# Optimization experiments

Measured on AMD Instinct MI355X. Metric: run time of the kernel, lower is better.

The kernel has to match this reference:

```python
import jax, jax.numpy as jnp
import numpy as np

H = 768          # hidden_size
V = 32000        # vocab_size
NUM_GATES = 5    # none/dontcare/ptr/yes/no
PAD = 0          # pad_token_id


def setup_inputs() -> dict:
    key = jax.random.key(0)
    ks = jax.random.split(key, 10)
    B, S, J, Ls = 16, 512, 30, 4
    max_len = 8
    sc = 1.0 / np.sqrt(H).astype(np.float32)
    E = jax.random.normal(ks[0], (V, H), jnp.float32) * sc
    E = E.at[PAD].set(0.0)  # padding_idx row is zero
    return dict(
        input_ids=jax.random.randint(ks[1], (B, S), 0, V),
        encoder_output=jax.random.normal(ks[2], (B, S, H), jnp.float32),
        hidden=jax.random.normal(ks[3], (1, B, H), jnp.float32),
        input_masks=jnp.ones((B, S), jnp.int32),  # 1 = valid token
        slot=jax.random.randint(ks[4], (J, Ls), 0, V),
        max_len=max_len,
        E=E,
        W_ih=jax.random.normal(ks[5], (3 * H, H), jnp.float32) * sc,
        W_hh=jax.random.normal(ks[6], (3 * H, H), jnp.float32) * sc,
        b_ih=jnp.zeros((3 * H,), jnp.float32),
        b_hh=jnp.zeros((3 * H,), jnp.float32),
        W_gen=jax.random.normal(ks[7], (3 * H, 1), jnp.float32) * sc,
        b_gen=jnp.zeros((1,), jnp.float32),
        W_gate=jax.random.normal(ks[8], (H, NUM_GATES), jnp.float32) * sc,
        b_gate=jnp.zeros((NUM_GATES,), jnp.float32),
    )


def gru_step(x, h, W_ih, W_hh, b_ih, b_hh):
    # PyTorch GRUCell math
    gi = x @ W_ih.T + b_ih
    gh = h @ W_hh.T + b_hh
    ir, iz, inn = jnp.split(gi, 3, axis=-1)
    hr, hz, hn = jnp.split(gh, 3, axis=-1)
    r = jax.nn.sigmoid(ir + hr)
    z = jax.nn.sigmoid(iz + hz)
    n = jnp.tanh(inn + r * hn)
    return (1.0 - z) * n + z * h


def reference(input_ids, encoder_output, hidden, input_masks, slot, max_len,
              E, W_ih, W_hh, b_ih, b_hh, W_gen, b_gen, W_gate, b_gate):
    B, S, Hd = encoder_output.shape
    J = slot.shape[0]
    mask = input_masks != 1                         # True -> masked (pad)
    slot_e = E[slot].sum(axis=1)                    # [J, H]
    BJ = B * J
    # parallel decoding: flat index = b*J + j (matches repeat/repeat_interleave)
    w = jnp.tile(slot_e, (B, 1))                    # [BJ, H]
    h = jnp.repeat(hidden[0], J, axis=0)            # [BJ, H]
    enc = jnp.repeat(encoder_output, J, axis=0)     # [BJ, S, H]
    ids = jnp.repeat(input_ids, J, axis=0)          # [BJ, S]
    msk = jnp.repeat(mask, J, axis=0)               # [BJ, S]
    rows = jnp.arange(BJ)

    def step(carry, _):
        w, h = carry
        h = gru_step(w, h, W_ih, W_hh, b_ih, b_hh)                    # [BJ, H]
        attn_e = jnp.einsum('bsh,bh->bs', enc, h)                     # [BJ, S]
        attn_e = jnp.where(msk, -1e9, attn_e)
        attn_history = jax.nn.softmax(attn_e, axis=-1)                # [BJ, S]
        attn_vocab = jax.nn.softmax(h @ E.T, axis=-1)                 # [BJ, V]
        context = jnp.einsum('bs,bsh->bh', attn_history, enc)         # [BJ, H]
        p_gen = jax.nn.sigmoid(
            jnp.concatenate([w, h, context], -1) @ W_gen + b_gen)     # [BJ, 1]
        ptr = jnp.zeros_like(attn_vocab).at[rows[:, None], ids].add(attn_history)
        p_final = p_gen * attn_vocab + (1.0 - p_gen) * ptr            # [BJ, V]
        w_next = E[jnp.argmax(p_final, axis=-1)]                      # greedy (teacher=None)
        return (w_next, h), (p_final, context)

    (_, _), (points, contexts) = jax.lax.scan(step, (w, h), None, length=max_len)
    gate_logit = contexts[0] @ W_gate + b_gate                        # gate from step k==0
    all_points = points.transpose(1, 0, 2).reshape(B, J, max_len, V)
    all_gates = gate_logit.reshape(B, J, NUM_GATES)
    return all_points, all_gates
```

## Files before the change

### kernel.cpp

```cpp
#include <hip/hip_runtime.h>
#include <cstdint>
#include <cstddef>

#define HDIM 768
#define VOCAB 32000
#define NGATES 5
#define NJ 30
#define NB 16
#define NS 512
#define NBJ (NB*NJ)
#define G3 2304
#define PR 608
#define NBV 250

typedef _Float16 f16;
typedef _Float16 f16x8 __attribute__((ext_vector_type(8)));
typedef float f32x4 __attribute__((ext_vector_type(4)));

#define GLOBAL_AS __attribute__((address_space(1)))
#define LDS_AS    __attribute__((address_space(3)))

__global__ void k_cast(const float* __restrict__ src, f16* __restrict__ dst, int n) {
    for (int i = blockIdx.x*256 + threadIdx.x; i < n; i += gridDim.x*256)
        dst[i] = (f16)src[i];
}

__global__ void k_cast_split(const float* __restrict__ src, f16* __restrict__ hi,
                             f16* __restrict__ lo, int n) {
    for (int i = blockIdx.x*256 + threadIdx.x; i < n; i += gridDim.x*256) {
        float v = src[i];
        f16 h = (f16)v;
        hi[i] = h;
        lo[i] = (f16)(v - (float)h);
    }
}

__global__ void k_init_state(const float* __restrict__ E, const int* __restrict__ slot,
                             const float* __restrict__ hidden,
                             f16* __restrict__ w_hi, f16* __restrict__ w_lo,
                             float* __restrict__ h,
                             f16* __restrict__ h_hi, f16* __restrict__ h_lo) {
    int total = NBJ*HDIM;
    for (int i = blockIdx.x*256 + threadIdx.x; i < total; i += gridDim.x*256) {
        int hh = i % HDIM, row = i / HDIM;
        int b = row / NJ, j = row % NJ;
        float s = 0.f;
        #pragma unroll
        for (int l = 0; l < 4; ++l) s += E[(long)slot[j*4+l]*HDIM + hh];
        f16 sh = (f16)s;
        w_hi[i] = sh; w_lo[i] = (f16)(s - (float)sh);
        float hv = hidden[b*HDIM + hh];
        h[i] = hv;
        f16 hh16 = (f16)hv;
        h_hi[i] = hh16; h_lo[i] = (f16)(hv - (float)hh16);
    }
}

__launch_bounds__(256)
__global__ void k_gemm(const f16* __restrict__ Ah, const f16* __restrict__ Al,
                       const f16* __restrict__ Bh, const f16* __restrict__ Bl,
                       float* __restrict__ Cf, f16* __restrict__ Ch,
                       float* __restrict__ psum,
                       int M, long ldc, long coff, int kdim, int nspan,
                       long aBS, long bBS, long cBS) {
    __shared__ f16 a_lds[8][128][8];
    __shared__ f16 b_lds[8][128][8];
    __shared__ float sbuf[2][128];

    const int tid = threadIdx.x;
    const int z = blockIdx.z;
    const int m0 = blockIdx.x*128, n0 = blockIdx.y*128;
    const int w = tid >> 6, lane = tid & 63;
    const int wm = (w >> 1)*64, wn = (w & 1)*64;
    const int lr = lane & 15, lg = lane >> 4;

    f32x4 acc[4][4] = {};

    for (int sp = 0; sp < nspan; ++sp) {
        const f16* Ap = ((sp < 2) ? Ah : Al) + (long)z*aBS;
        const f16* Bp = ((sp == 1) ? Bl : Bh) + (long)z*bBS;
        for (int kc = 0; kc < kdim; kc += 64) {
            #pragma unroll
            for (int i = 0; i < 4; ++i) {
                const int idx = w*4 + i;
                const int c = idx >> 1;
                const int rl = (idx & 1)*64 + lane;
                const f16* ga = Ap + (long)(m0 + rl)*kdim + kc + c*8;
                const f16* gb = Bp + (long)(n0 + rl)*kdim + kc + c*8;
                __builtin_amdgcn_global_load_lds(
                    (const GLOBAL_AS unsigned int*)ga,
                    (LDS_AS unsigned int*)((char*)&a_lds[0][0][0] + idx*1024), 16, 0, 0);
                __builtin_amdgcn_global_load_lds(
                    (const GLOBAL_AS unsigned int*)gb,
                    (LDS_AS unsigned int*)((char*)&b_lds[0][0][0] + idx*1024), 16, 0, 0);
            }
            __syncthreads();
            #pragma unroll
            for (int kk = 0; kk < 2; ++kk) {
                const int c = kk*4 + lg;
                f16x8 af[4], bf[4];
                #pragma unroll
                for (int mi = 0; mi < 4; ++mi) af[mi] = *(const f16x8*)&a_lds[c][wm + mi*16 + lr][0];
                #pragma unroll
                for (int nf = 0; nf < 4; ++nf) bf[nf] = *(const f16x8*)&b_lds[c][wn + nf*16 + lr][0];
                #pragma unroll
                for (int mi = 0; mi < 4; ++mi)
                    #pragma unroll
                    for (int nf = 0; nf < 4; ++nf)
                        acc[mi][nf] = __builtin_amdgcn_mfma_f32_16x16x32_f16(af[mi], bf[nf], acc[mi][nf], 0, 0, 0);
            }
            __syncthreads();
        }
    }

    if (Ch != nullptr) {
        f16* Cb = Ch + (long)z*cBS + coff;
        #pragma unroll
        for (int mi = 0; mi < 4; ++mi)
            #pragma unroll
            for (int nf = 0; nf < 4; ++nf) {
                int col = n0 + wn + nf*16 + lr;
                int rowb = m0 + wm + mi*16 + lg*4;
                #pragma unroll
                for (int r = 0; r < 4; ++r) {
                    int row = rowb + r;
                    if (row < M) Cb[(long)row*ldc + col] = (f16)acc[mi][nf][r];
                }
            }
    } else {
        float* Cb = Cf + (long)z*cBS + coff;
        #pragma unroll
        for (int mi = 0; mi < 4; ++mi)
            #pragma unroll
            for (int nf = 0; nf < 4; ++nf) {
                int col = n0 + wn + nf*16 + lr;
                int rowb = m0 + wm + mi*16 + lg*4;
                #pragma unroll
                for (int r = 0; r < 4; ++r) {
                    int row = rowb + r;
                    if (row < M) Cb[(long)row*ldc + col] = acc[mi][nf][r];
                }
            }
    }

    if (psum != nullptr) {
        #pragma unroll
        for (int mi = 0; mi < 4; ++mi) {
            #pragma unroll
            for (int r = 0; r < 4; ++r) {
                float s = 0.f;
                #pragma unroll
                for (int nf = 0; nf < 4; ++nf) s += expf((float)(f16)acc[mi][nf][r]);
                s += __shfl_xor(s, 1); s += __shfl_xor(s, 2);
                s += __shfl_xor(s, 4); s += __shfl_xor(s, 8);
                if (lr == 0) sbuf[w & 1][wm + mi*16 + lg*4 + r] = s;
            }
        }
        __syncthreads();
        if (tid < 128)
            psum[(long)blockIdx.y*512 + m0 + tid] = sbuf[0][tid] + sbuf[1][tid];
    }
}

__global__ void k_gru_elem(const float* __restrict__ gi, const float* __restrict__ gh,
                           const float* __restrict__ bih, const float* __restrict__ bhh,
                           float* __restrict__ h, f16* __restrict__ h_hi, f16* __restrict__ h_lo) {
    int total = NBJ*HDIM;
    for (int i = blockIdx.x*256 + threadIdx.x; i < total; i += gridDim.x*256) {
        int c = i % HDIM; long row = i / HDIM;
        long base = row*G3;
        float r = gi[base + c]        + bih[c]        + gh[base + c]        + bhh[c];
        float z = gi[base + 768 + c]  + bih[768 + c]  + gh[base + 768 + c]  + bhh[768 + c];
        float hn = gh[base + 1536 + c] + bhh[1536 + c];
        float in_ = gi[base + 1536 + c] + bih[1536 + c];
        r = 1.f/(1.f + expf(-r));
        z = 1.f/(1.f + expf(-z));
        float n = tanhf(in_ + r*hn);
        float hv = (1.f - z)*n + z*h[i];
        h[i] = hv;
        f16 hh16 = (f16)hv;
        h_hi[i] = hh16; h_lo[i] = (f16)(hv - (float)hh16);
    }
}

__launch_bounds__(256)
__global__ void k_attn(const float* __restrict__ h, const float* __restrict__ enc,
                       float* __restrict__ attn_e) {
    __shared__ float h_lds[NJ][64];
    __shared__ float e_lds[64][65];
    const int b = blockIdx.x, st = blockIdx.y;
    const int s0 = st*64;
    const int tid = threadIdx.x;
    const int s = tid & 63, jg = tid >> 6;
    float acc[8] = {};
    for (int kc = 0; kc < HDIM; kc += 64) {
        for (int idx = tid; idx < NJ*64; idx += 256) {
            int j = idx >> 6, k = idx & 63;
            h_lds[j][k] = h[((long)(b*NJ + j))*HDIM + kc + k];
        }
        #pragma unroll
        for (int i = 0; i < 4; ++i) {
            int id = tid + i*256;
            int ss = id >> 4, kq = (id & 15)*4;
            float4 v = *(const float4*)&enc[((long)b*NS + s0 + ss)*HDIM + kc + kq];
            e_lds[ss][kq+0] = v.x; e_lds[ss][kq+1] = v.y;
            e_lds[ss][kq+2] = v.z; e_lds[ss][kq+3] = v.w;
        }
        __syncthreads();
        for (int k = 0; k < 64; ++k) {
            float e = e_lds[s][k];
            #pragma unroll
            for (int i = 0; i < 8; ++i) {
                int j = jg + i*4;
                if (j < NJ) acc[i] += h_lds[j][k]*e;
            }
        }
        __syncthreads();
    }
    #pragma unroll
    for (int i = 0; i < 8; ++i) {
        int j = jg + i*4;
        if (j < NJ) attn_e[((long)(b*NJ + j))*NS + s0 + s] = acc[i];
    }
}

__launch_bounds__(256)
__global__ void k_softmax_s(float* __restrict__ ae, const int* __restrict__ masks) {
    const int row = blockIdx.x, tid = threadIdx.x;
    const int b = row / NJ;
    __shared__ float red[256];
    float x0 = ae[(long)row*NS + tid];
    float x1 = ae[(long)row*NS + tid + 256];
    if (masks[b*NS + tid]       != 1) x0 = -1e9f;
    if (masks[b*NS + tid + 256] != 1) x1 = -1e9f;
    red[tid] = fmaxf(x0, x1); __syncthreads();
    for (int o = 128; o > 0; o >>= 1) { if (tid < o) red[tid] = fmaxf(red[tid], red[tid+o]); __syncthreads(); }
    float m = red[0]; __syncthreads();
    float e0 = expf(x0 - m), e1 = expf(x1 - m);
    red[tid] = e0 + e1; __syncthreads();
    for (int o = 128; o > 0; o >>= 1) { if (tid < o) red[tid] += red[tid+o]; __syncthreads(); }
    float inv = 1.f/red[0];
    ae[(long)row*NS + tid]       = e0*inv;
    ae[(long)row*NS + tid + 256] = e1*inv;
}

__launch_bounds__(256)
__global__ void k_context(const float* __restrict__ ah, const float* __restrict__ enc,
                          float* __restrict__ ctx) {
    __shared__ float a_lds[NJ][64];
    const int b = blockIdx.x, ht = blockIdx.y;
    const int hh = ht*128 + (threadIdx.x & 127);
    const int jg = threadIdx.x >> 7;
    float acc[15] = {};
    for (int sc = 0; sc < NS; sc += 64) {
        for (int idx = threadIdx.x; idx < NJ*64; idx += 256) {
            int j = idx >> 6, s = idx & 63;
            a_lds[j][s] = ah[((long)(b*NJ + j))*NS + sc + s];
        }
        __syncthreads();
        for (int s = 0; s < 64; ++s) {
            float e = enc[((long)b*NS + sc + s)*HDIM + hh];
            #pragma unroll
            for (int i = 0; i < 15; ++i) acc[i] += a_lds[jg + i*2][s]*e;
        }
        __syncthreads();
    }
    #pragma unroll
    for (int i = 0; i < 15; ++i) ctx[((long)(b*NJ + jg + i*2))*HDIM + hh] = acc[i];
}

__launch_bounds__(64)
__global__ void k_pgen(const f16* __restrict__ w_hi, const f16* __restrict__ w_lo,
                       const float* __restrict__ h,
                       const float* __restrict__ ctx, const float* __restrict__ Wgen,
                       const float* __restrict__ bgen, const float* __restrict__ Wgate,
                       const float* __restrict__ bgate, float* __restrict__ pgen,
                       float* __restrict__ out_gates, int do_gate) {
    const int row = blockIdx.x, lane = threadIdx.x;
    float acc = 0.f;
    for (int x = lane; x < HDIM; x += 64) {
        float wv = (float)w_hi[(long)row*HDIM + x] + (float)w_lo[(long)row*HDIM + x];
        acc += wv                          * Wgen[x];
        acc += h[(long)row*HDIM + x]       * Wgen[768 + x];
        acc += ctx[(long)row*HDIM + x]     * Wgen[1536 + x];
    }
    for (int o = 32; o > 0; o >>= 1) acc += __shfl_down(acc, o);
    if (lane == 0) pgen[row] = 1.f/(1.f + expf(-(acc + bgen[0])));
    if (do_gate) {
        for (int g = 0; g < NGATES; ++g) {
            float a = 0.f;
            for (int x = lane; x < HDIM; x += 64) a += ctx[(long)row*HDIM + x]*Wgate[x*NGATES + g];
            for (int o = 32; o > 0; o >>= 1) a += __shfl_down(a, o);
            if (lane == 0) out_gates[row*NGATES + g] = a + bgate[g];
        }
    }
}

__launch_bounds__(256)
__global__ void k_scale(const f16* __restrict__ l16, float* __restrict__ out,
                        long ldrow, long coff,
                        const float* __restrict__ psum, const float* __restrict__ pgen,
                        unsigned long long* __restrict__ pamax) {
    const int row = blockIdx.x, c = blockIdx.y, tid = threadIdx.x;
    __shared__ float red[256];
    float s = 0.f;
    for (int nb = tid; nb < NBV; nb += 256) s += psum[(long)nb*512 + row];
    red[tid] = s; __syncthreads();
    for (int o = 128; o > 0; o >>= 1) { if (tid < o) red[tid] += red[tid+o]; __syncthreads(); }
    const float scale = pgen[row] / red[0];

    const f16* lb = l16 + (long)row*VOCAB;
    float* ob = out + (long)row*ldrow + coff;
    const int v0 = c*4000;
    float bv = -1.f; int bi = 0x7FFFFFFF;
    for (int v = v0 + tid; v < v0 + 4000; v += 256) {
        float val = scale*expf((float)lb[v]);
        ob[v] = val;
        if (val > bv) { bv = val; bi = v; }
    }
    __shared__ float rv[256]; __shared__ int ri[256];
    rv[tid] = bv; ri[tid] = bi; __syncthreads();
    for (int o = 128; o > 0; o >>= 1) {
        if (tid < o) {
            float v2 = rv[tid+o]; int i2 = ri[tid+o];
            if (v2 > rv[tid] || (v2 == rv[tid] && i2 < ri[tid])) { rv[tid] = v2; ri[tid] = i2; }
        }
        __syncthreads();
    }
    if (tid == 0)
        pamax[(long)row*8 + c] = ((unsigned long long)__float_as_uint(rv[0]) << 32)
                               | (unsigned long long)(0xFFFFFFFFu - (unsigned)ri[0]);
}

__launch_bounds__(256)
__global__ void k_scatter(float* __restrict__ pts, long ldrow, long coff,
                          const int* __restrict__ ids, const float* __restrict__ ah,
                          const float* __restrict__ pgen,
                          const unsigned long long* __restrict__ pamax,
                          const float* __restrict__ E,
                          f16* __restrict__ w_hi, f16* __restrict__ w_lo) {
    const int row = blockIdx.x, tid = threadIdx.x;
    const int b = row / NJ;
    float* base = pts + (long)row*ldrow + coff;
    const float cp = 1.f - pgen[row];
    float sv = -1.f; int si = 0x7FFFFFFF;
    for (int ss = tid; ss < NS; ss += 256) {
        int id = ids[(long)b*NS + ss];
        float add = cp * ah[(long)row*NS + ss];
        float old = atomicAdd(base + id, add);
        float cand = old + add;
        if (cand > sv || (cand == sv && id < si)) { sv = cand; si = id; }
    }
    __shared__ float rv[256]; __shared__ int ri[256];
    rv[tid] = sv; ri[tid] = si; __syncthreads();
    for (int o = 128; o > 0; o >>= 1) {
        if (tid < o) {
            float v2 = rv[tid+o]; int i2 = ri[tid+o];
            if (v2 > rv[tid] || (v2 == rv[tid] && i2 < ri[tid])) { rv[tid] = v2; ri[tid] = i2; }
        }
        __syncthreads();
    }
    __shared__ int bidx;
    if (tid == 0) {
        float vv = rv[0]; int ii = ri[0];
        #pragma unroll
        for (int cc = 0; cc < 8; ++cc) {
            unsigned long long pk = pamax[(long)row*8 + cc];
            float pv = __uint_as_float((unsigned)(pk >> 32));
            int pi = (int)(0xFFFFFFFFu - (unsigned)(pk & 0xFFFFFFFFu));
            if (pv > vv || (pv == vv && pi < ii)) { vv = pv; ii = pi; }
        }
        bidx = ii;
    }
    __syncthreads();
    const int idx = bidx;
    for (int x = tid; x < HDIM; x += 256) {
        float ev = E[(long)idx*HDIM + x];
        f16 eh = (f16)ev;
        w_hi[(long)row*HDIM + x] = eh;
        w_lo[(long)row*HDIM + x] = (f16)(ev - (float)eh);
    }
}

extern "C" void kernel_launch(void* const* d_in, const int* in_sizes, int n_in,
                              void* d_out, int out_size, void* d_ws, size_t ws_size,
                              hipStream_t stream) {
    const int*   input_ids = (const int*)  d_in[0];
    const float* enc       = (const float*)d_in[1];
    const float* hidden    = (const float*)d_in[2];
    const int*   masks     = (const int*)  d_in[3];
    const int*   slot      = (const int*)  d_in[4];
    const float* E     = (const float*)d_in[6];
    const float* Wih   = (const float*)d_in[7];
    const float* Whh   = (const float*)d_in[8];
    const float* bih   = (const float*)d_in[9];
    const float* bhh   = (const float*)d_in[10];
    const float* Wgen  = (const float*)d_in[11];
    const float* bgen  = (const float*)d_in[12];
    const float* Wgate = (const float*)d_in[13];
    const float* bgate = (const float*)d_in[14];

    const int ml = (out_size / NBJ - NGATES) / VOCAB;
    float* out = (float*)d_out;
    float* gates_out = out + (long)NBJ*ml*VOCAB;

    char* ws = (char*)d_ws;
    auto carve = [&](size_t bytes) { char* p = ws; ws += (bytes + 255) & ~(size_t)255; return p; };
    f16*   E16   = (f16*)carve((size_t)VOCAB*HDIM*2);
    f16*   WH2   = (f16*)carve((size_t)2*G3*HDIM*2);
    f16*   WL2   = (f16*)carve((size_t)2*G3*HDIM*2);
    f16*   SH    = (f16*)carve((size_t)2*PR*HDIM*2);
    f16*   SL    = (f16*)carve((size_t)2*PR*HDIM*2);
    float* gigh  = (float*)carve((size_t)2*NBJ*G3*4);
    float* hbuf  = (float*)carve((size_t)NBJ*HDIM*4);
    float* ae    = (float*)carve((size_t)NBJ*NS*4);
    float* ctx   = (float*)carve((size_t)NBJ*HDIM*4);
    f16*   l16   = (f16*)carve((size_t)NBJ*VOCAB*2);
    float* pgen  = (float*)carve((size_t)NBJ*4);
    float* ps    = (float*)carve((size_t)NBV*512*4);
    unsigned long long* pamax = (unsigned long long*)carve((size_t)NBJ*8*8);

    f16* WihH = WH2;  f16* WihL = WL2;
    f16* wH = SH;     f16* wL = SL;
    f16* hH = SH + (size_t)PR*HDIM;
    f16* hL = SL + (size_t)PR*HDIM;

    k_cast<<<8192, 256, 0, stream>>>(E, E16, VOCAB*HDIM);
    k_cast_split<<<2048, 256, 0, stream>>>(Wih, WihH, WihL, G3*HDIM);
    k_cast_split<<<2048, 256, 0, stream>>>(Whh, WH2 + (size_t)G3*HDIM, WL2 + (size_t)G3*HDIM, G3*HDIM);
    k_init_state<<<1440, 256, 0, stream>>>(E, slot, hidden, wH, wL, hbuf, hH, hL);

    const long ldrow = (long)ml*VOCAB;
    for (int t = 0; t < ml; ++t) {
        k_gemm<<<dim3(4, 18, 2), 256, 0, stream>>>(wH, wL, WihH, WihL, gigh, nullptr, nullptr,
            NBJ, (long)G3, 0, HDIM, 3, (long)PR*HDIM, (long)G3*HDIM, (long)NBJ*G3);
        k_gru_elem<<<1440, 256, 0, stream>>>(gigh, gigh + (size_t)NBJ*G3, bih, bhh, hbuf, hH, hL);
        k_attn<<<dim3(NB, 8), 256, 0, stream>>>(hbuf, enc, ae);
        k_softmax_s<<<NBJ, 256, 0, stream>>>(ae, masks);
        k_context<<<dim3(NB, 6), 256, 0, stream>>>(ae, enc, ctx);
        k_pgen<<<NBJ, 64, 0, stream>>>(wH, wL, hbuf, ctx, Wgen, bgen, Wgate, bgate,
                                       pgen, gates_out, t == 0 ? 1 : 0);
        k_gemm<<<dim3(4, NBV, 1), 256, 0, stream>>>(hH, hL, E16, nullptr, nullptr, l16, ps,
            NBJ, (long)VOCAB, 0, HDIM, 1, 0, 0, 0);
        k_scale<<<dim3(NBJ, 8), 256, 0, stream>>>(l16, out, ldrow, (long)t*VOCAB, ps, pgen, pamax);
        k_scatter<<<NBJ, 256, 0, stream>>>(out, ldrow, (long)t*VOCAB, input_ids, ae, pgen,
                                           pamax, E, wH, wL);
    }
}
```

Baseline: 3.409 ms.

## Fuse all per-step kernels into one persistent kernel with grid barriers

Replaces the sequence of roughly nine kernel launches per decode step, plus the setup casts, with a single persistent kernel. It is sized to the occupancy-limited grid and separates phases with an atomic-counter global barrier. Work items (GEMM tiles, attention tiles, rows) are distributed round-robin over the resident blocks, and LDS is shared through a union. The goal is to remove launch overhead and inter-kernel gaps. In exchange, every phase is limited to the resident block count, each phase costs a global barrier spin, and the scale and scatter kernels are merged into one row loop.

```diff
diff --git a/kernel.cpp b/kernel.cpp
--- a/kernel.cpp
+++ b/kernel.cpp
@@ -14,62 +14,40 @@
 #define NBV 250
 
 typedef _Float16 f16;
+typedef _Float16 f16x4 __attribute__((ext_vector_type(4)));
 typedef _Float16 f16x8 __attribute__((ext_vector_type(8)));
 typedef float f32x4 __attribute__((ext_vector_type(4)));
 
 #define GLOBAL_AS __attribute__((address_space(1)))
 #define LDS_AS    __attribute__((address_space(3)))
 
-__global__ void k_cast(const float* __restrict__ src, f16* __restrict__ dst, int n) {
-    for (int i = blockIdx.x*256 + threadIdx.x; i < n; i += gridDim.x*256)
-        dst[i] = (f16)src[i];
+union SharedU {
+    struct { f16 a[8][128][8]; f16 b[8][128][8]; float sbuf[2][128]; } g;
+    struct { float h[NJ][64]; float e[64][65]; } at;
+    struct { float a[NJ][64]; } cx;
+    struct { float red[256]; float rv[256]; int ri[256]; } rd;
+};
+
+__device__ __forceinline__ void gbar(unsigned* bar, unsigned nblk, unsigned& ph) {
+    __syncthreads();
+    ph += nblk;
+    if (threadIdx.x == 0) {
+        __threadfence();
+        __hip_atomic_fetch_add(bar, 1u, __ATOMIC_RELEASE, __HIP_MEMORY_SCOPE_AGENT);
+        while (__hip_atomic_load(bar, __ATOMIC_ACQUIRE, __HIP_MEMORY_SCOPE_AGENT) < ph)
+            __builtin_amdgcn_s_sleep(2);
+        __threadfence();
+    }
+    __syncthreads();
 }
 
-__global__ void k_cast_split(const float* __restrict__ src, f16* __restrict__ hi,
-                             f16* __restrict__ lo, int n) {
-    for (int i = blockIdx.x*256 + threadIdx.x; i < n; i += gridDim.x*256) {
-        float v = src[i];
-        f16 h = (f16)v;
-        hi[i] = h;
-        lo[i] = (f16)(v - (float)h);
-    }
-}
-
-__global__ void k_init_state(const float* __restrict__ E, const int* __restrict__ slot,
-                             const float* __restrict__ hidden,
-                             f16* __restrict__ w_hi, f16* __restrict__ w_lo,
-                             float* __restrict__ h,
-                             f16* __restrict__ h_hi, f16* __restrict__ h_lo) {
-    int total = NBJ*HDIM;
-    for (int i = blockIdx.x*256 + threadIdx.x; i < total; i += gridDim.x*256) {
-        int hh = i % HDIM, row = i / HDIM;
-        int b = row / NJ, j = row % NJ;
-        float s = 0.f;
-        #pragma unroll
-        for (int l = 0; l < 4; ++l) s += E[(long)slot[j*4+l]*HDIM + hh];
-        f16 sh = (f16)s;
-        w_hi[i] = sh; w_lo[i] = (f16)(s - (float)sh);
-        float hv = hidden[b*HDIM + hh];
-        h[i] = hv;
-        f16 hh16 = (f16)hv;
-        h_hi[i] = hh16; h_lo[i] = (f16)(hv - (float)hh16);
-    }
-}
-
-__launch_bounds__(256)
-__global__ void k_gemm(const f16* __restrict__ Ah, const f16* __restrict__ Al,
-                       const f16* __restrict__ Bh, const f16* __restrict__ Bl,
-                       float* __restrict__ Cf, f16* __restrict__ Ch,
-                       float* __restrict__ psum,
-                       int M, long ldc, long coff, int kdim, int nspan,
-                       long aBS, long bBS, long cBS) {
-    __shared__ f16 a_lds[8][128][8];
-    __shared__ f16 b_lds[8][128][8];
-    __shared__ float sbuf[2][128];
-
+__device__ __forceinline__ void gemm_tile(
+        const f16* __restrict__ Ah, const f16* __restrict__ Al,
+        const f16* __restrict__ Bh, const f16* __restrict__ Bl,
+        float* __restrict__ Cf, f16* __restrict__ Ch, float* __restrict__ psum,
+        int M, long ldc, int kdim, int nspan, int bx, int by, SharedU* sh) {
     const int tid = threadIdx.x;
-    const int z = blockIdx.z;
-    const int m0 = blockIdx.x*128, n0 = blockIdx.y*128;
+    const int m0 = bx*128, n0 = by*128;
     const int w = tid >> 6, lane = tid & 63;
     const int wm = (w >> 1)*64, wn = (w & 1)*64;
     const int lr = lane & 15, lg = lane >> 4;
@@ -77,8 +55,8 @@
     f32x4 acc[4][4] = {};
 
     for (int sp = 0; sp < nspan; ++sp) {
-        const f16* Ap = ((sp < 2) ? Ah : Al) + (long)z*aBS;
-        const f16* Bp = ((sp == 1) ? Bl : Bh) + (long)z*bBS;
+        const f16* Ap = (sp < 2) ? Ah : Al;
+        const f16* Bp = (sp == 1) ? Bl : Bh;
         for (int kc = 0; kc < kdim; kc += 64) {
             #pragma unroll
             for (int i = 0; i < 4; ++i) {
@@ -89,10 +67,10 @@
                 const f16* gb = Bp + (long)(n0 + rl)*kdim + kc + c*8;
                 __builtin_amdgcn_global_load_lds(
                     (const GLOBAL_AS unsigned int*)ga,
-                    (LDS_AS unsigned int*)((char*)&a_lds[0][0][0] + idx*1024), 16, 0, 0);
+                    (LDS_AS unsigned int*)((char*)&sh->g.a[0][0][0] + idx*1024), 16, 0, 0);
                 __builtin_amdgcn_global_load_lds(
                     (const GLOBAL_AS unsigned int*)gb,
-                    (LDS_AS unsigned int*)((char*)&b_lds[0][0][0] + idx*1024), 16, 0, 0);
+                    (LDS_AS unsigned int*)((char*)&sh->g.b[0][0][0] + idx*1024), 16, 0, 0);
             }
             __syncthreads();
             #pragma unroll
@@ -100,9 +78,9 @@
                 const int c = kk*4 + lg;
                 f16x8 af[4], bf[4];
                 #pragma unroll
-                for (int mi = 0; mi < 4; ++mi) af[mi] = *(const f16x8*)&a_lds[c][wm + mi*16 + lr][0];
-                #pragma unroll
-                for (int nf = 0; nf < 4; ++nf) bf[nf] = *(const f16x8*)&b_lds[c][wn + nf*16 + lr][0];
+                for (int mi = 0; mi < 4; ++mi) af[mi] = *(const f16x8*)&sh->g.a[c][wm + mi*16 + lr][0];
+                #pragma unroll
+                for (int nf = 0; nf < 4; ++nf) bf[nf] = *(const f16x8*)&sh->g.b[c][wn + nf*16 + lr][0];
                 #pragma unroll
                 for (int mi = 0; mi < 4; ++mi)
                     #pragma unroll
@@ -114,7 +92,6 @@
     }
 
     if (Ch != nullptr) {
-        f16* Cb = Ch + (long)z*cBS + coff;
         #pragma unroll
         for (int mi = 0; mi < 4; ++mi)
             #pragma unroll
@@ -124,11 +101,10 @@
                 #pragma unroll
                 for (int r = 0; r < 4; ++r) {
                     int row = rowb + r;
-                    if (row < M) Cb[(long)row*ldc + col] = (f16)acc[mi][nf][r];
+                    if (row < M) Ch[(long)row*ldc + col] = (f16)acc[mi][nf][r];
                 }
             }
     } else {
-        float* Cb = Cf + (long)z*cBS + coff;
         #pragma unroll
         for (int mi = 0; mi < 4; ++mi)
             #pragma unroll
@@ -138,7 +114,7 @@
                 #pragma unroll
                 for (int r = 0; r < 4; ++r) {
                     int row = rowb + r;
-                    if (row < M) Cb[(long)row*ldc + col] = acc[mi][nf][r];
+                    if (row < M) Cf[(long)row*ldc + col] = acc[mi][nf][r];
                 }
             }
     }
@@ -153,232 +129,274 @@
                 for (int nf = 0; nf < 4; ++nf) s += expf((float)(f16)acc[mi][nf][r]);
                 s += __shfl_xor(s, 1); s += __shfl_xor(s, 2);
                 s += __shfl_xor(s, 4); s += __shfl_xor(s, 8);
-                if (lr == 0) sbuf[w & 1][wm + mi*16 + lg*4 + r] = s;
+                if (lr == 0) sh->g.sbuf[w & 1][wm + mi*16 + lg*4 + r] = s;
             }
         }
         __syncthreads();
-        if (tid < 128)
-            psum[(long)blockIdx.y*512 + m0 + tid] = sbuf[0][tid] + sbuf[1][tid];
+        if (tid < 128) psum[(long)by*512 + m0 + tid] = sh->g.sbuf[0][tid] + sh->g.sbuf[1][tid];
+        __syncthreads();
     }
 }
 
-__global__ void k_gru_elem(const float* __restrict__ gi, const float* __restrict__ gh,
-                           const float* __restrict__ bih, const float* __restrict__ bhh,
-                           float* __restrict__ h, f16* __restrict__ h_hi, f16* __restrict__ h_lo) {
-    int total = NBJ*HDIM;
-    for (int i = blockIdx.x*256 + threadIdx.x; i < total; i += gridDim.x*256) {
-        int c = i % HDIM; long row = i / HDIM;
-        long base = row*G3;
-        float r = gi[base + c]        + bih[c]        + gh[base + c]        + bhh[c];
-        float z = gi[base + 768 + c]  + bih[768 + c]  + gh[base + 768 + c]  + bhh[768 + c];
-        float hn = gh[base + 1536 + c] + bhh[1536 + c];
-        float in_ = gi[base + 1536 + c] + bih[1536 + c];
-        r = 1.f/(1.f + expf(-r));
-        z = 1.f/(1.f + expf(-z));
-        float n = tanhf(in_ + r*hn);
-        float hv = (1.f - z)*n + z*h[i];
-        h[i] = hv;
-        f16 hh16 = (f16)hv;
-        h_hi[i] = hh16; h_lo[i] = (f16)(hv - (float)hh16);
-    }
-}
-
-__launch_bounds__(256)
-__global__ void k_attn(const float* __restrict__ h, const float* __restrict__ enc,
-                       float* __restrict__ attn_e) {
-    __shared__ float h_lds[NJ][64];
-    __shared__ float e_lds[64][65];
-    const int b = blockIdx.x, st = blockIdx.y;
-    const int s0 = st*64;
-    const int tid = threadIdx.x;
-    const int s = tid & 63, jg = tid >> 6;
-    float acc[8] = {};
-    for (int kc = 0; kc < HDIM; kc += 64) {
-        for (int idx = tid; idx < NJ*64; idx += 256) {
-            int j = idx >> 6, k = idx & 63;
-            h_lds[j][k] = h[((long)(b*NJ + j))*HDIM + kc + k];
-        }
-        #pragma unroll
-        for (int i = 0; i < 4; ++i) {
-            int id = tid + i*256;
-            int ss = id >> 4, kq = (id & 15)*4;
-            float4 v = *(const float4*)&enc[((long)b*NS + s0 + ss)*HDIM + kc + kq];
-            e_lds[ss][kq+0] = v.x; e_lds[ss][kq+1] = v.y;
-            e_lds[ss][kq+2] = v.z; e_lds[ss][kq+3] = v.w;
-        }
-        __syncthreads();
-        for (int k = 0; k < 64; ++k) {
-            float e = e_lds[s][k];
+__launch_bounds__(256, 2)
+__global__ void k_mega(const int* __restrict__ ids, const float* __restrict__ enc,
+                       const float* __restrict__ hidden, const int* __restrict__ masks,
+                       const int* __restrict__ slot, const float* __restrict__ E,
+                       const float* __restrict__ Wih, const float* __restrict__ Whh,
+                       const float* __restrict__ bih, const float* __restrict__ bhh,
+                       const float* __restrict__ Wgen, const float* __restrict__ bgen,
+                       const float* __restrict__ Wgate, const float* __restrict__ bgate,
+                       float* __restrict__ out, float* __restrict__ gates_out, int ml,
+                       f16* __restrict__ E16, f16* __restrict__ WH2, f16* __restrict__ WL2,
+                       f16* __restrict__ SH, f16* __restrict__ SL,
+                       float* __restrict__ gigh, float* __restrict__ hbuf,
+                       float* __restrict__ ae, float* __restrict__ ctx,
+                       f16* __restrict__ l16, float* __restrict__ pgen,
+                       float* __restrict__ ps, unsigned* __restrict__ bar, int nblk) {
+    __shared__ SharedU sh;
+    __shared__ int s_bidx;
+    unsigned ph = 0;
+
+    const int blk = blockIdx.x, tid = threadIdx.x;
+    f16* wH = SH;                       f16* wL = SL;
+    f16* hH = SH + (size_t)PR*HDIM;     f16* hL = SL + (size_t)PR*HDIM;
+    float* gi = gigh;                   float* gh = gigh + (size_t)NBJ*G3;
+    const long ldrow = (long)ml*VOCAB;
+
+    {
+        const long nE = (long)VOCAB*HDIM;
+        for (long i = (long)(blk*256 + tid)*4; i < nE; i += (long)nblk*256*4) {
+            float4 v = *(const float4*)&E[i];
+            f16x4 o = { (f16)v.x, (f16)v.y, (f16)v.z, (f16)v.w };
+            *(f16x4*)&E16[i] = o;
+        }
+        const long nW = (long)G3*HDIM;
+        for (long i = (long)(blk*256 + tid)*4; i < nW; i += (long)nblk*256*4) {
+            float4 a = *(const float4*)&Wih[i];
+            f16x4 h = { (f16)a.x, (f16)a.y, (f16)a.z, (f16)a.w };
+            f16x4 l = { (f16)(a.x-(float)h[0]), (f16)(a.y-(float)h[1]),
+                        (f16)(a.z-(float)h[2]), (f16)(a.w-(float)h[3]) };
+            *(f16x4*)&WH2[i] = h; *(f16x4*)&WL2[i] = l;
+            float4 b = *(const float4*)&Whh[i];
+            f16x4 h2 = { (f16)b.x, (f16)b.y, (f16)b.z, (f16)b.w };
+            f16x4 l2 = { (f16)(b.x-(float)h2[0]), (f16)(b.y-(float)h2[1]),
+                         (f16)(b.z-(float)h2[2]), (f16)(b.w-(float)h2[3]) };
+            *(f16x4*)&WH2[nW + i] = h2; *(f16x4*)&WL2[nW + i] = l2;
+        }
+        for (int i = blk*256 + tid; i < NBJ*HDIM; i += nblk*256) {
+            int hh = i % HDIM, row = i / HDIM;
+            int b = row / NJ, j = row % NJ;
+            float s = 0.f;
+            #pragma unroll
+            for (int l = 0; l < 4; ++l) s += E[(long)slot[j*4+l]*HDIM + hh];
+            f16 sh16 = (f16)s;
+            wH[i] = sh16; wL[i] = (f16)(s - (float)sh16);
+            float hv = hidden[b*HDIM + hh];
+            hbuf[i] = hv;
+            f16 hh16 = (f16)hv;
+            hH[i] = hh16; hL[i] = (f16)(hv - (float)hh16);
+        }
+    }
+    gbar(bar, nblk, ph);
+
+    for (int t = 0; t < ml; ++t) {
+        for (int bi = blk; bi < 144; bi += nblk) {
+            int z = bi / 72, r = bi % 72, bx = r & 3, by = r >> 2;
+            gemm_tile(z ? hH : wH, z ? hL : wL,
+                      WH2 + (size_t)z*G3*HDIM, WL2 + (size_t)z*G3*HDIM,
+                      z ? gh : gi, nullptr, nullptr,
+                      NBJ, (long)G3, HDIM, 3, bx, by, &sh);
+        }
+        gbar(bar, nblk, ph);
+
+        for (int i = blk*256 + tid; i < NBJ*HDIM; i += nblk*256) {
+            int c = i % HDIM; long row = i / HDIM;
+            long base = row*G3;
+            float r = gi[base + c]         + bih[c]        + gh[base + c]         + bhh[c];
+            float z = gi[base + 768 + c]   + bih[768 + c]  + gh[base + 768 + c]   + bhh[768 + c];
+            float hn  = gh[base + 1536 + c] + bhh[1536 + c];
+            float in_ = gi[base + 1536 + c] + bih[1536 + c];
+            r = 1.f/(1.f + expf(-r));
+            z = 1.f/(1.f + expf(-z));
+            float n = tanhf(in_ + r*hn);
+            float hv = (1.f - z)*n + z*hbuf[i];
+            hbuf[i] = hv;
+            f16 hh16 = (f16)hv;
+            hH[i] = hh16; hL[i] = (f16)(hv - (float)hh16);
+        }
+        gbar(bar, nblk, ph);
+
+        for (int bi = blk; bi < 128; bi += nblk) {
+            __syncthreads();
+            const int b = bi >> 3, s0 = (bi & 7)*64;
+            const int s = tid & 63, jg = tid >> 6;
+            float acc[8] = {};
+            for (int kc = 0; kc < HDIM; kc += 64) {
+                for (int idx = tid; idx < NJ*64; idx += 256) {
+                    int j = idx >> 6, k = idx & 63;
+                    sh.at.h[j][k] = hbuf[((long)(b*NJ + j))*HDIM + kc + k];
+                }
+                #pragma unroll
+                for (int i = 0; i < 4; ++i) {
+                    int id = tid + i*256;
+                    int ss = id >> 4, kq = (id & 15)*4;
+                    float4 v = *(const float4*)&enc[((long)b*NS + s0 + ss)*HDIM + kc + kq];
+                    sh.at.e[ss][kq+0] = v.x; sh.at.e[ss][kq+1] = v.y;
+                    sh.at.e[ss][kq+2] = v.z; sh.at.e[ss][kq+3] = v.w;
+                }
+                __syncthreads();
+                for (int k = 0; k < 64; ++k) {
+                    float e = sh.at.e[s][k];
+                    #pragma unroll
+                    for (int i = 0; i < 8; ++i) {
+                        int j = jg + i*4;
+                        if (j < NJ) acc[i] += sh.at.h[j][k]*e;
+                    }
+                }
+                __syncthreads();
+            }
             #pragma unroll
             for (int i = 0; i < 8; ++i) {
                 int j = jg + i*4;
-                if (j < NJ) acc[i] += h_lds[j][k]*e;
-            }
-        }
-        __syncthreads();
-    }
-    #pragma unroll
-    for (int i = 0; i < 8; ++i) {
-        int j = jg + i*4;
-        if (j < NJ) attn_e[((long)(b*NJ + j))*NS + s0 + s] = acc[i];
-    }
-}
-
-__launch_bounds__(256)
-__global__ void k_softmax_s(float* __restrict__ ae, const int* __restrict__ masks) {
-    const int row = blockIdx.x, tid = threadIdx.x;
-    const int b = row / NJ;
-    __shared__ float red[256];
-    float x0 = ae[(long)row*NS + tid];
-    float x1 = ae[(long)row*NS + tid + 256];
-    if (masks[b*NS + tid]       != 1) x0 = -1e9f;
-    if (masks[b*NS + tid + 256] != 1) x1 = -1e9f;
-    red[tid] = fmaxf(x0, x1); __syncthreads();
-    for (int o = 128; o > 0; o >>= 1) { if (tid < o) red[tid] = fmaxf(red[tid], red[tid+o]); __syncthreads(); }
-    float m = red[0]; __syncthreads();
-    float e0 = expf(x0 - m), e1 = expf(x1 - m);
-    red[tid] = e0 + e1; __syncthreads();
-    for (int o = 128; o > 0; o >>= 1) { if (tid < o) red[tid] += red[tid+o]; __syncthreads(); }
-    float inv = 1.f/red[0];
-    ae[(long)row*NS + tid]       = e0*inv;
-    ae[(long)row*NS + tid + 256] = e1*inv;
-}
-
-__launch_bounds__(256)
-__global__ void k_context(const float* __restrict__ ah, const float* __restrict__ enc,
-                          float* __restrict__ ctx) {
-    __shared__ float a_lds[NJ][64];
-    const int b = blockIdx.x, ht = blockIdx.y;
-    const int hh = ht*128 + (threadIdx.x & 127);
-    const int jg = threadIdx.x >> 7;
-    float acc[15] = {};
-    for (int sc = 0; sc < NS; sc += 64) {
-        for (int idx = threadIdx.x; idx < NJ*64; idx += 256) {
-            int j = idx >> 6, s = idx & 63;
-            a_lds[j][s] = ah[((long)(b*NJ + j))*NS + sc + s];
-        }
-        __syncthreads();
-        for (int s = 0; s < 64; ++s) {
-            float e = enc[((long)b*NS + sc + s)*HDIM + hh];
-            #pragma unroll
-            for (int i = 0; i < 15; ++i) acc[i] += a_lds[jg + i*2][s]*e;
-        }
-        __syncthreads();
-    }
-    #pragma unroll
-    for (int i = 0; i < 15; ++i) ctx[((long)(b*NJ + jg + i*2))*HDIM + hh] = acc[i];
-}
-
-__launch_bounds__(64)
-__global__ void k_pgen(const f16* __restrict__ w_hi, const f16* __restrict__ w_lo,
-                       const float* __restrict__ h,
-                       const float* __restrict__ ctx, const float* __restrict__ Wgen,
-                       const float* __restrict__ bgen, const float* __restrict__ Wgate,
-                       const float* __restrict__ bgate, float* __restrict__ pgen,
-                       float* __restrict__ out_gates, int do_gate) {
-    const int row = blockIdx.x, lane = threadIdx.x;
-    float acc = 0.f;
-    for (int x = lane; x < HDIM; x += 64) {
-        float wv = (float)w_hi[(long)row*HDIM + x] + (float)w_lo[(long)row*HDIM + x];
-        acc += wv                          * Wgen[x];
-        acc += h[(long)row*HDIM + x]       * Wgen[768 + x];
-        acc += ctx[(long)row*HDIM + x]     * Wgen[1536 + x];
-    }
-    for (int o = 32; o > 0; o >>= 1) acc += __shfl_down(acc, o);
-    if (lane == 0) pgen[row] = 1.f/(1.f + expf(-(acc + bgen[0])));
-    if (do_gate) {
-        for (int g = 0; g < NGATES; ++g) {
-            float a = 0.f;
-            for (int x = lane; x < HDIM; x += 64) a += ctx[(long)row*HDIM + x]*Wgate[x*NGATES + g];
-            for (int o = 32; o > 0; o >>= 1) a += __shfl_down(a, o);
-            if (lane == 0) out_gates[row*NGATES + g] = a + bgate[g];
-        }
-    }
-}
-
-__launch_bounds__(256)
-__global__ void k_scale(const f16* __restrict__ l16, float* __restrict__ out,
-                        long ldrow, long coff,
-                        const float* __restrict__ psum, const float* __restrict__ pgen,
-                        unsigned long long* __restrict__ pamax) {
-    const int row = blockIdx.x, c = blockIdx.y, tid = threadIdx.x;
-    __shared__ float red[256];
-    float s = 0.f;
-    for (int nb = tid; nb < NBV; nb += 256) s += psum[(long)nb*512 + row];
-    red[tid] = s; __syncthreads();
-    for (int o = 128; o > 0; o >>= 1) { if (tid < o) red[tid] += red[tid+o]; __syncthreads(); }
-    const float scale = pgen[row] / red[0];
-
-    const f16* lb = l16 + (long)row*VOCAB;
-    float* ob = out + (long)row*ldrow + coff;
-    const int v0 = c*4000;
-    float bv = -1.f; int bi = 0x7FFFFFFF;
-    for (int v = v0 + tid; v < v0 + 4000; v += 256) {
-        float val = scale*expf((float)lb[v]);
-        ob[v] = val;
-        if (val > bv) { bv = val; bi = v; }
-    }
-    __shared__ float rv[256]; __shared__ int ri[256];
-    rv[tid] = bv; ri[tid] = bi; __syncthreads();
-    for (int o = 128; o > 0; o >>= 1) {
-        if (tid < o) {
-            float v2 = rv[tid+o]; int i2 = ri[tid+o];
-            if (v2 > rv[tid] || (v2 == rv[tid] && i2 < ri[tid])) { rv[tid] = v2; ri[tid] = i2; }
-        }
-        __syncthreads();
-    }
-    if (tid == 0)
-        pamax[(long)row*8 + c] = ((unsigned long long)__float_as_uint(rv[0]) << 32)
-                               | (unsigned long long)(0xFFFFFFFFu - (unsigned)ri[0]);
-}
-
-__launch_bounds__(256)
-__global__ void k_scatter(float* __restrict__ pts, long ldrow, long coff,
-                          const int* __restrict__ ids, const float* __restrict__ ah,
-                          const float* __restrict__ pgen,
-                          const unsigned long long* __restrict__ pamax,
-                          const float* __restrict__ E,
-                          f16* __restrict__ w_hi, f16* __restrict__ w_lo) {
-    const int row = blockIdx.x, tid = threadIdx.x;
-    const int b = row / NJ;
-    float* base = pts + (long)row*ldrow + coff;
-    const float cp = 1.f - pgen[row];
-    float sv = -1.f; int si = 0x7FFFFFFF;
-    for (int ss = tid; ss < NS; ss += 256) {
-        int id = ids[(long)b*NS + ss];
-        float add = cp * ah[(long)row*NS + ss];
-        float old = atomicAdd(base + id, add);
-        float cand = old + add;
-        if (cand > sv || (cand == sv && id < si)) { sv = cand; si = id; }
-    }
-    __shared__ float rv[256]; __shared__ int ri[256];
-    rv[tid] = sv; ri[tid] = si; __syncthreads();
-    for (int o = 128; o > 0; o >>= 1) {
-        if (tid < o) {
-            float v2 = rv[tid+o]; int i2 = ri[tid+o];
-            if (v2 > rv[tid] || (v2 == rv[tid] && i2 < ri[tid])) { rv[tid] = v2; ri[tid] = i2; }
-        }
-        __syncthreads();
-    }
-    __shared__ int bidx;
-    if (tid == 0) {
-        float vv = rv[0]; int ii = ri[0];
-        #pragma unroll
-        for (int cc = 0; cc < 8; ++cc) {
-            unsigned long long pk = pamax[(long)row*8 + cc];
-            float pv = __uint_as_float((unsigned)(pk >> 32));
-            int pi = (int)(0xFFFFFFFFu - (unsigned)(pk & 0xFFFFFFFFu));
-            if (pv > vv || (pv == vv && pi < ii)) { vv = pv; ii = pi; }
-        }
-        bidx = ii;
-    }
-    __syncthreads();
-    const int idx = bidx;
-    for (int x = tid; x < HDIM; x += 256) {
-        float ev = E[(long)idx*HDIM + x];
-        f16 eh = (f16)ev;
-        w_hi[(long)row*HDIM + x] = eh;
-        w_lo[(long)row*HDIM + x] = (f16)(ev - (float)eh);
+                if (j < NJ) ae[((long)(b*NJ + j))*NS + s0 + s] = acc[i];
+            }
+        }
+        gbar(bar, nblk, ph);
+
+        for (int row = blk; row < NBJ; row += nblk) {
+            __syncthreads();
+            const int b = row / NJ;
+            float x0 = ae[(long)row*NS + tid];
+            float x1 = ae[(long)row*NS + tid + 256];
+            if (masks[b*NS + tid]       != 1) x0 = -1e9f;
+            if (masks[b*NS + tid + 256] != 1) x1 = -1e9f;
+            sh.rd.red[tid] = fmaxf(x0, x1); __syncthreads();
+            for (int o = 128; o > 0; o >>= 1) { if (tid < o) sh.rd.red[tid] = fmaxf(sh.rd.red[tid], sh.rd.red[tid+o]); __syncthreads(); }
+            float m = sh.rd.red[0]; __syncthreads();
+            float e0 = expf(x0 - m), e1 = expf(x1 - m);
+            sh.rd.red[tid] = e0 + e1; __syncthreads();
+            for (int o = 128; o > 0; o >>= 1) { if (tid < o) sh.rd.red[tid] += sh.rd.red[tid+o]; __syncthreads(); }
+            float inv = 1.f/sh.rd.red[0];
+            ae[(long)row*NS + tid]       = e0*inv;
+            ae[(long)row*NS + tid + 256] = e1*inv;
+        }
+        gbar(bar, nblk, ph);
+
+        for (int bi = blk; bi < 96; bi += nblk) {
+            __syncthreads();
+            const int b = bi / 6, ht = bi % 6;
+            const int hh = ht*128 + (tid & 127);
+            const int jg = tid >> 7;
+            float acc[15] = {};
+            for (int sc = 0; sc < NS; sc += 64) {
+                for (int idx = tid; idx < NJ*64; idx += 256) {
+                    int j = idx >> 6, s = idx & 63;
+                    sh.cx.a[j][s] = ae[((long)(b*NJ + j))*NS + sc + s];
+                }
+                __syncthreads();
+                for (int s = 0; s < 64; ++s) {
+                    float e = enc[((long)b*NS + sc + s)*HDIM + hh];
+                    #pragma unroll
+                    for (int i = 0; i < 15; ++i) acc[i] += sh.cx.a[jg + i*2][s]*e;
+                }
+                __syncthreads();
+            }
+            #pragma unroll
+            for (int i = 0; i < 15; ++i) ctx[((long)(b*NJ + jg + i*2))*HDIM + hh] = acc[i];
+        }
+        gbar(bar, nblk, ph);
+
+        for (int row = blk; row < NBJ; row += nblk) {
+            __syncthreads();
+            float acc = 0.f;
+            for (int x = tid; x < HDIM; x += 256) {
+                float wv = (float)wH[(long)row*HDIM + x] + (float)wL[(long)row*HDIM + x];
+                acc += wv*Wgen[x] + hbuf[(long)row*HDIM + x]*Wgen[768 + x]
+                     + ctx[(long)row*HDIM + x]*Wgen[1536 + x];
+            }
+            sh.rd.red[tid] = acc; __syncthreads();
+            for (int o = 128; o > 0; o >>= 1) { if (tid < o) sh.rd.red[tid] += sh.rd.red[tid+o]; __syncthreads(); }
+            if (tid == 0) pgen[row] = 1.f/(1.f + expf(-(sh.rd.red[0] + bgen[0])));
+            if (t == 0) {
+                for (int g = 0; g < NGATES; ++g) {
+                    __syncthreads();
+                    float a = 0.f;
+                    for (int x = tid; x < HDIM; x += 256) a += ctx[(long)row*HDIM + x]*Wgate[x*NGATES + g];
+                    sh.rd.red[tid] = a; __syncthreads();
+                    for (int o = 128; o > 0; o >>= 1) { if (tid < o) sh.rd.red[tid] += sh.rd.red[tid+o]; __syncthreads(); }
+                    if (tid == 0) gates_out[row*NGATES + g] = sh.rd.red[0] + bgate[g];
+                }
+            }
+        }
+        gbar(bar, nblk, ph);
+
+        for (int vt = blk; vt < 4*NBV; vt += nblk) {
+            gemm_tile(hH, nullptr, E16, nullptr, nullptr, l16, ps,
+                      NBJ, (long)VOCAB, HDIM, 1, vt & 3, vt >> 2, &sh);
+        }
+        gbar(bar, nblk, ph);
+
+        for (int row = blk; row < NBJ; row += nblk) {
+            __syncthreads();
+            const int b = row / NJ;
+            float* base = out + (long)row*ldrow + (long)t*VOCAB;
+            const f16* lb = l16 + (long)row*VOCAB;
+            float s = 0.f;
+            for (int nb = tid; nb < NBV; nb += 256) s += ps[(long)nb*512 + row];
+            sh.rd.red[tid] = s; __syncthreads();
+            for (int o = 128; o > 0; o >>= 1) { if (tid < o) sh.rd.red[tid] += sh.rd.red[tid+o]; __syncthreads(); }
+            const float pg = pgen[row];
+            const float scale = pg / sh.rd.red[0];
+
+            float bv = -1.f; int bi = 0;
+            for (int v = tid; v < VOCAB; v += 256) {
+                float val = scale*expf((float)lb[v]);
+                base[v] = val;
+                if (val > bv) { bv = val; bi = v; }
+            }
+            sh.rd.rv[tid] = bv; sh.rd.ri[tid] = bi; __syncthreads();
+            for (int o = 128; o > 0; o >>= 1) {
+                if (tid < o) {
+                    float v2 = sh.rd.rv[tid+o]; int i2 = sh.rd.ri[tid+o];
+                    if (v2 > sh.rd.rv[tid] || (v2 == sh.rd.rv[tid] && i2 < sh.rd.ri[tid])) { sh.rd.rv[tid] = v2; sh.rd.ri[tid] = i2; }
+                }
+                __syncthreads();
+            }
+            float v0 = sh.rd.rv[0]; int i0 = sh.rd.ri[0];
+            __syncthreads();
+
+            const float cp = 1.f - pg;
+            float sv = -1.f; int si = 0x7FFFFFFF;
+            for (int ss = tid; ss < NS; ss += 256) {
+                int id = ids[(long)b*NS + ss];
+                float add = cp * ae[(long)row*NS + ss];
+                float old = atomicAdd(base + id, add);
+                float cand = old + add;
+                if (cand > sv || (cand == sv && id < si)) { sv = cand; si = id; }
+            }
+            sh.rd.rv[tid] = sv; sh.rd.ri[tid] = si; __syncthreads();
+            for (int o = 128; o > 0; o >>= 1) {
+                if (tid < o) {
+                    float v2 = sh.rd.rv[tid+o]; int i2 = sh.rd.ri[tid+o];
+                    if (v2 > sh.rd.rv[tid] || (v2 == sh.rd.rv[tid] && i2 < sh.rd.ri[tid])) { sh.rd.rv[tid] = v2; sh.rd.ri[tid] = i2; }
+                }
+                __syncthreads();
+            }
+            if (tid == 0) {
+                float vv = v0; int ii = i0;
+                if (sh.rd.rv[0] > vv || (sh.rd.rv[0] == vv && sh.rd.ri[0] < ii)) { vv = sh.rd.rv[0]; ii = sh.rd.ri[0]; }
+                s_bidx = ii;
+            }
+            __syncthreads();
+            const int idx = s_bidx;
+            for (int x = tid; x < HDIM; x += 256) {
+                float ev = E[(long)idx*HDIM + x];
+                f16 eh = (f16)ev;
+                wH[(long)row*HDIM + x] = eh;
+                wL[(long)row*HDIM + x] = (f16)(ev - (float)eh);
+            }
+        }
+        gbar(bar, nblk, ph);
     }
 }
 
@@ -400,12 +418,13 @@
     const float* Wgate = (const float*)d_in[13];
     const float* bgate = (const float*)d_in[14];
 
-    const int ml = (out_size / NBJ - NGATES) / VOCAB;
+    int ml = (out_size / NBJ - NGATES) / VOCAB;
     float* out = (float*)d_out;
     float* gates_out = out + (long)NBJ*ml*VOCAB;
 
     char* ws = (char*)d_ws;
     auto carve = [&](size_t bytes) { char* p = ws; ws += (bytes + 255) & ~(size_t)255; return p; };
+    unsigned* bar = (unsigned*)carve(256);
     f16*   E16   = (f16*)carve((size_t)VOCAB*HDIM*2);
     f16*   WH2   = (f16*)carve((size_t)2*G3*HDIM*2);
     f16*   WL2   = (f16*)carve((size_t)2*G3*HDIM*2);
@@ -418,32 +437,18 @@
     f16*   l16   = (f16*)carve((size_t)NBJ*VOCAB*2);
     float* pgen  = (float*)carve((size_t)NBJ*4);
     float* ps    = (float*)carve((size_t)NBV*512*4);
-    unsigned long long* pamax = (unsigned long long*)carve((size_t)NBJ*8*8);
-
-    f16* WihH = WH2;  f16* WihL = WL2;
-    f16* wH = SH;     f16* wL = SL;
-    f16* hH = SH + (size_t)PR*HDIM;
-    f16* hL = SL + (size_t)PR*HDIM;
-
-    k_cast<<<8192, 256, 0, stream>>>(E, E16, VOCAB*HDIM);
-    k_cast_split<<<2048, 256, 0, stream>>>(Wih, WihH, WihL, G3*HDIM);
-    k_cast_split<<<2048, 256, 0, stream>>>(Whh, WH2 + (size_t)G3*HDIM, WL2 + (size_t)G3*HDIM, G3*HDIM);
-    k_init_state<<<1440, 256, 0, stream>>>(E, slot, hidden, wH, wL, hbuf, hH, hL);
-
-    const long ldrow = (long)ml*VOCAB;
-    for (int t = 0; t < ml; ++t) {
-        k_gemm<<<dim3(4, 18, 2), 256, 0, stream>>>(wH, wL, WihH, WihL, gigh, nullptr, nullptr,
-            NBJ, (long)G3, 0, HDIM, 3, (long)PR*HDIM, (long)G3*HDIM, (long)NBJ*G3);
-        k_gru_elem<<<1440, 256, 0, stream>>>(gigh, gigh + (size_t)NBJ*G3, bih, bhh, hbuf, hH, hL);
-        k_attn<<<dim3(NB, 8), 256, 0, stream>>>(hbuf, enc, ae);
-        k_softmax_s<<<NBJ, 256, 0, stream>>>(ae, masks);
-        k_context<<<dim3(NB, 6), 256, 0, stream>>>(ae, enc, ctx);
-        k_pgen<<<NBJ, 64, 0, stream>>>(wH, wL, hbuf, ctx, Wgen, bgen, Wgate, bgate,
-                                       pgen, gates_out, t == 0 ? 1 : 0);
-        k_gemm<<<dim3(4, NBV, 1), 256, 0, stream>>>(hH, hL, E16, nullptr, nullptr, l16, ps,
-            NBJ, (long)VOCAB, 0, HDIM, 1, 0, 0, 0);
-        k_scale<<<dim3(NBJ, 8), 256, 0, stream>>>(l16, out, ldrow, (long)t*VOCAB, ps, pgen, pamax);
-        k_scatter<<<NBJ, 256, 0, stream>>>(out, ldrow, (long)t*VOCAB, input_ids, ae, pgen,
-                                           pamax, E, wH, wL);
-    }
+
+    int dev = 0; (void)hipGetDevice(&dev);
+    int ncu = 0; (void)hipDeviceGetAttribute(&ncu, hipDeviceAttributeMultiprocessorCount, dev);
+    int occ = 0; (void)hipOccupancyMaxActiveBlocksPerMultiprocessor(&occ, (const void*)k_mega, 256, 0);
+    if (ncu <= 0) ncu = 256;
+    if (occ <= 0) occ = 1;
+    long cap = (long)occ * (long)ncu;
+    int nblk = (int)(cap < 512 ? cap : 512);
+
+    (void)hipMemsetAsync(bar, 0, sizeof(unsigned), stream);
+    k_mega<<<dim3(nblk), dim3(256), 0, stream>>>(
+        input_ids, enc, hidden, masks, slot, E, Wih, Whh, bih, bhh,
+        Wgen, bgen, Wgate, bgate, out, gates_out, ml,
+        E16, WH2, WL2, SH, SL, gigh, hbuf, ae, ctx, l16, pgen, ps, bar, nblk);
 }
```

Result: slower. 13.03 ms (+282.3%).
